# Optimization experiments

Measured on AMD Instinct MI355X. Metric: run time of the kernel, lower is better.

## Reference

```python
import jax, jax.numpy as jnp
import numpy as np

EPS = 1e-12
BIG_NEG = 1e10
SPARSE_RATIO = 0.5
ATTN_W = 0.8
KEEPED = 39          # int(196 * 0.4 * 0.5)
HIDDEN = 102         # int(512 * 0.2)
DIM = 512


def l2norm(x, axis=-1):
    n = jnp.sqrt(jnp.sum(x * x, axis=axis, keepdims=True))
    return x / jnp.maximum(n, EPS)


def layernorm(x, g, b):
    mu = jnp.mean(x, axis=-1, keepdims=True)
    var = jnp.mean(jnp.square(x - mu), axis=-1, keepdims=True)
    return (x - mu) / jnp.sqrt(var + 1e-5) * g + b


def token_aggregation(x, ln_g, ln_b, W1, b1, W2, b2, scale):
    # x: [B, L, C] -> [B, K, C]
    h = layernorm(x, ln_g, ln_b)
    h = jax.nn.gelu(h @ W1 + b1, approximate=False)
    w = h @ W2 + b2                       # [B, L, K]
    w = jnp.swapaxes(w, 1, 2) * scale     # [B, K, L]
    w = jax.nn.softmax(w, axis=2)
    return jnp.einsum('bkl,blc->bkc', w, x)


def setup_inputs() -> dict:
    key = jax.random.key(0)
    ks = jax.random.split(key, 8)
    B_v, L_v, B_t, L_t = 256, 197, 256, 64
    inp = {
        'img_embs': jax.random.normal(ks[0], (B_v, L_v, DIM), jnp.float32),
        'cap_embs': jax.random.normal(ks[1], (B_t, L_t, DIM), jnp.float32),
        'cap_lens': jax.random.randint(ks[2], (B_t,), 8, L_t + 1),
        'ln_g': jnp.ones((DIM,), jnp.float32),
        'ln_b': jnp.zeros((DIM,), jnp.float32),
        'W1': jax.random.normal(ks[3], (DIM, HIDDEN), jnp.float32) * 0.02,
        'b1': jnp.zeros((HIDDEN,), jnp.float32),
        'W2': jax.random.normal(ks[4], (HIDDEN, KEEPED), jnp.float32) * 0.02,
        'b2': jnp.zeros((KEEPED,), jnp.float32),
        'scale': jnp.ones((1, 1, 1), jnp.float32),
    }
    return inp


def reference(img_embs, cap_embs, cap_lens, ln_g, ln_b, W1, b1, W2, b2, scale):
    B_v = img_embs.shape[0]
    L_t = cap_embs.shape[1]
    num_keep = int(KEEPED * SPARSE_RATIO)  # 19

    # CLS split (197 is not a perfect square -> has_cls_token)
    img_cls = img_embs[:, 0:1, :]
    spatial = img_embs[:, 1:, :]

    aggr = token_aggregation(spatial, ln_g, ln_b, W1, b1, W2, b2, scale)  # [B_v, 39, C]
    aggr_norm = l2norm(aggr)
    cap_norm = l2norm(cap_embs)

    glo = jax.lax.stop_gradient(l2norm(jnp.mean(aggr, axis=1, keepdims=True)))
    att_self = jax.lax.stop_gradient(jnp.sum(glo * aggr_norm, axis=-1))  # [B_v, 39]

    word_mask = (jnp.arange(L_t)[None, :] < cap_lens[:, None]).astype(img_embs.dtype)

    def one_caption(cap_i, cap_i_norm, m):
        nw = jnp.sum(m)
        cap_glo = jax.lax.stop_gradient(
            l2norm(jnp.sum(cap_i * m[:, None], axis=0) / nw))        # [C]
        att_y = jax.lax.stop_gradient(
            jnp.sum(cap_glo * aggr_norm, axis=-1))                    # [B_v, 39]
        score = ATTN_W * att_y + (1.0 - ATTN_W) * att_self
        _, idx = jax.lax.top_k(score, num_keep)                       # [B_v, 19]
        select = jnp.take_along_axis(aggr, idx[:, :, None], axis=1)   # [B_v, 19, C]
        score_mask = jnp.zeros_like(score).at[
            jnp.arange(B_v)[:, None], idx].set(1.0)                   # [B_v, 39]
        w_drop = jax.nn.softmax(score - score_mask * BIG_NEG, axis=-1)
        extra = jnp.einsum('bl,blc->bc', w_drop, aggr)[:, None, :]    # [B_v, 1, C]
        sel = l2norm(jnp.concatenate([img_cls, select, extra], axis=1))  # [B_v, 21, C]
        sim = jnp.einsum('wc,bkc->bwk', cap_i_norm, sel)              # [B_v, L_t, 21]
        sim_max = jnp.max(sim, axis=-1)                               # [B_v, L_t]
        sim_text = jnp.sum(sim_max * m, axis=-1) / nw                 # [B_v]
        return sim_text, score_mask

    sims, score_mask_all = jax.vmap(one_caption)(cap_embs, cap_norm, word_mask)
    return sims.T  # [B_v, B_t]
```

## Files before the change

### kernel.cpp

```cpp
#include <hip/hip_runtime.h>
#include <hip/hip_bf16.h>
#include <cfloat>
#include <cmath>

typedef float f32x4 __attribute__((ext_vector_type(4)));
typedef float f32x2 __attribute__((ext_vector_type(2)));
typedef short bf16x8 __attribute__((ext_vector_type(8)));

#define HID 102
#define KEEPN 39
#define DIMD 512

static __device__ __forceinline__ unsigned int f2bf(float v) {
  unsigned int b = __float_as_uint(v);
  return (b + 0x7FFFu + ((b >> 16) & 1u)) >> 16;
}
static __device__ __forceinline__ float wsum(float v) {
#pragma unroll
  for (int m = 1; m < 64; m <<= 1) v += __shfl_xor(v, m, 64);
  return v;
}
static __device__ __forceinline__ float wmaxr(float v) {
#pragma unroll
  for (int m = 1; m < 64; m <<= 1) v = fmaxf(v, __shfl_xor(v, m, 64));
  return v;
}
static __device__ __forceinline__ float bsum(float v, float* red4, int lane, int wid) {
  v = wsum(v);
  if (lane == 0) red4[wid] = v;
  __syncthreads();
  float r = red4[0] + red4[1] + red4[2] + red4[3];
  __syncthreads();
  return r;
}

__global__ __launch_bounds__(256) void k0_prep(
    const float* __restrict__ W1, const float* __restrict__ b1,
    const float* __restrict__ W2, const float* __restrict__ lng,
    const float* __restrict__ lnb,
    float* __restrict__ w1gT, float* __restrict__ b1eff, float* __restrict__ w2T) {
  int tid = blockIdx.x * 256 + threadIdx.x;
  for (int idx = tid; idx < HID * DIMD; idx += (int)gridDim.x * 256) {
    int c = idx >> 9, k = idx & 511;
    w1gT[idx] = lng[k] * W1[k * HID + c];
  }
  for (int idx = tid; idx < KEEPN * 104; idx += (int)gridDim.x * 256) {
    int l = idx / 104, k = idx - l * 104;
    w2T[idx] = (k < HID) ? W2[k * KEEPN + l] : 0.0f;
  }
  if (blockIdx.x == 0 && threadIdx.x < 104) {
    int c = threadIdx.x;
    float s = 0.f;
    if (c < HID) {
      s = b1[c];
      for (int k = 0; k < DIMD; ++k) s += lnb[k] * W1[k * HID + c];
    }
    b1eff[c] = s;
  }
}

__global__ __launch_bounds__(256, 2) void k1a(
    const float* __restrict__ img, const float* __restrict__ w1gT,
    const float* __restrict__ b1eff, const float* __restrict__ w2T,
    const float* __restrict__ b2, const float* __restrict__ scale,
    float* __restrict__ wmat) {
  int b = blockIdx.x;
  int tid = threadIdx.x;
  int lane = tid & 63, wid = tid >> 6;
  __shared__ float mu_s[196], rs_s[196];
  __shared__ __attribute__((aligned(16))) float w2t_s[KEEPN * 104];
  __shared__ float b1e_s[104];
  __shared__ __attribute__((aligned(16))) float uni[6864];
  float* x_s = uni;
  float* w1g_s = uni + 2176;
  float* h1_s = uni;
  const float* xb = img + (size_t)b * 197 * DIMD + DIMD;
  float scv = scale[0];
  for (int u = tid; u < KEEPN * 104 / 4; u += 256)
    ((f32x4*)w2t_s)[u] = ((const f32x4*)w2T)[u];
  if (tid < 104) b1e_s[tid] = b1eff[tid];
#pragma unroll 1
  for (int it = 0; it < 49; ++it) {
    int t = it * 4 + wid;
    const float* xr = xb + (size_t)t * DIMD + lane * 8;
    f32x4 v0 = *(const f32x4*)xr;
    f32x4 v1 = *(const f32x4*)(xr + 4);
    float s = v0[0]+v0[1]+v0[2]+v0[3]+v1[0]+v1[1]+v1[2]+v1[3];
    float q = v0[0]*v0[0]+v0[1]*v0[1]+v0[2]*v0[2]+v0[3]*v0[3]
            + v1[0]*v1[0]+v1[1]*v1[1]+v1[2]*v1[2]+v1[3]*v1[3];
    s = wsum(s); q = wsum(q);
    if (lane == 0) {
      float mu = s * (1.f/512.f);
      float var = q * (1.f/512.f) - mu*mu;
      mu_s[t] = mu;
      rs_s[t] = 1.f / sqrtf(var + 1e-5f);
    }
  }
  __syncthreads();
  int kh = tid >> 7, r = tid & 127, tg = r & 15, cg = r >> 4;
#pragma unroll 1
  for (int t0 = 0; t0 < 196; t0 += 64) {
    float acc[4][13] = {};
#pragma unroll 1
    for (int kc = 0; kc < DIMD; kc += 32) {
      __syncthreads();
#pragma unroll
      for (int j = 0; j < 2; ++j) {
        int u = tid + 256 * j;
        int tt = u >> 3, f = u & 7;
        int t = t0 + tt;
        if (t < 196) {
          f32x4 v = *(const f32x4*)(xb + (size_t)t * DIMD + kc + 4*f);
          float mu = mu_s[t], rs = rs_s[t];
          x_s[(4*f+0)*68 + tt] = (v[0]-mu)*rs;
          x_s[(4*f+1)*68 + tt] = (v[1]-mu)*rs;
          x_s[(4*f+2)*68 + tt] = (v[2]-mu)*rs;
          x_s[(4*f+3)*68 + tt] = (v[3]-mu)*rs;
        }
      }
#pragma unroll
      for (int j = 0; j < 4; ++j) {
        int u = tid + 256 * j;
        if (u < 816) {
          int c = u >> 3, f = u & 7;
          *(f32x4*)&w1g_s[c*36 + 4*f] = *(const f32x4*)(w1gT + c*DIMD + kc + 4*f);
        }
      }
      __syncthreads();
#pragma unroll
      for (int k4 = 0; k4 < 4; ++k4) {
        int kk = kh*16 + k4*4;
        f32x4 a0 = *(const f32x4*)&x_s[(kk+0)*68 + 4*tg];
        f32x4 a1 = *(const f32x4*)&x_s[(kk+1)*68 + 4*tg];
        f32x4 a2 = *(const f32x4*)&x_s[(kk+2)*68 + 4*tg];
        f32x4 a3 = *(const f32x4*)&x_s[(kk+3)*68 + 4*tg];
#pragma unroll
        for (int ci = 0; ci < 13; ++ci) {
          f32x4 w = *(const f32x4*)&w1g_s[(cg*13+ci)*36 + kk];
#pragma unroll
          for (int t = 0; t < 4; ++t)
            acc[t][ci] += a0[t]*w[0] + a1[t]*w[1] + a2[t]*w[2] + a3[t]*w[3];
        }
      }
    }
    __syncthreads();
    if (kh == 1) {
#pragma unroll
      for (int ci = 0; ci < 13; ++ci) {
        int c = cg*13 + ci;
        if (c < HID)
#pragma unroll
          for (int t = 0; t < 4; ++t) h1_s[c*66 + 4*tg + t] = acc[t][ci];
      }
    }
    __syncthreads();
    if (kh == 0) {
#pragma unroll
      for (int ci = 0; ci < 13; ++ci) {
        int c = cg*13 + ci;
        if (c < HID)
#pragma unroll
          for (int t = 0; t < 4; ++t) {
            float v = h1_s[c*66 + 4*tg + t] + acc[t][ci] + b1e_s[c];
            v = 0.5f * v * (1.f + erff(v * 0.70710678118654752f));
            h1_s[c*66 + 4*tg + t] = v;
          }
      }
    }
    if (tid < 128) h1_s[(HID + (tid >> 6))*66 + (tid & 63)] = 0.f;
    __syncthreads();
    {
      int t4 = tid & 31, lg = tid >> 5;
      int nl = (lg == 7) ? 4 : 5;
      float a2c[2][5] = {};
#pragma unroll 2
      for (int k = 0; k < 104; k += 4) {
        f32x4 wvv[5];
#pragma unroll
        for (int li = 0; li < 5; ++li) {
          if (li < nl) wvv[li] = *(const f32x4*)&w2t_s[(lg*5+li)*104 + k];
          else wvv[li] = (f32x4){0.f,0.f,0.f,0.f};
        }
#pragma unroll
        for (int j = 0; j < 4; ++j) {
          f32x2 h = *(const f32x2*)&h1_s[(k+j)*66 + 2*t4];
#pragma unroll
          for (int li = 0; li < 5; ++li) {
            a2c[0][li] += h[0]*wvv[li][j];
            a2c[1][li] += h[1]*wvv[li][j];
          }
        }
      }
#pragma unroll
      for (int li = 0; li < 5; ++li) {
        if (li < nl) {
          int l = lg*5 + li;
          float bb = b2[l];
#pragma unroll
          for (int tp = 0; tp < 2; ++tp) {
            int t = t0 + 2*t4 + tp;
            if (t < 196) wmat[((size_t)b*KEEPN + l)*196 + t] = (a2c[tp][li] + bb) * scv;
          }
        }
      }
    }
  }
}

__global__ __launch_bounds__(256) void k1agg(
    const float* __restrict__ img, const float* __restrict__ wmat,
    float* __restrict__ agn, unsigned short* __restrict__ bm,
    float* __restrict__ na_g, float* __restrict__ gloraw) {
  int b = blockIdx.x, tid = threadIdx.x;
  int lane = tid & 63, wid = tid >> 6;
  __shared__ __attribute__((aligned(16))) float wm_s[KEEPN * 200];
  __shared__ float red_s[13 * 4];
  __shared__ float na_s[13];
  for (int u = tid; u < KEEPN * 49; u += 256) {
    int l = u / 49, t4 = u - l * 49;
    *(f32x4*)&wm_s[l*200 + 4*t4] = *(const f32x4*)(wmat + ((size_t)b*KEEPN + l)*196 + 4*t4);
  }
  __syncthreads();
  for (int l = wid; l < KEEPN; l += 4) {
    float v0 = wm_s[l*200 + lane];
    float v1 = wm_s[l*200 + 64 + lane];
    float v2 = wm_s[l*200 + 128 + lane];
    float v3 = (lane < 4) ? wm_s[l*200 + 192 + lane] : -FLT_MAX;
    float mx = wmaxr(fmaxf(fmaxf(v0, v1), fmaxf(v2, v3)));
    float e0 = expf(v0 - mx), e1 = expf(v1 - mx), e2 = expf(v2 - mx);
    float e3 = (lane < 4) ? expf(v3 - mx) : 0.f;
    float s = wsum(e0 + e1 + e2 + e3);
    float inv = 1.f / s;
    wm_s[l*200 + lane] = e0 * inv;
    wm_s[l*200 + 64 + lane] = e1 * inv;
    wm_s[l*200 + 128 + lane] = e2 * inv;
    if (lane < 4) wm_s[l*200 + 192 + lane] = e3 * inv;
  }
  __syncthreads();
  const float* xb = img + (size_t)b * 197 * DIMD + DIMD;
  int cc = 2 * tid;
  float ms0 = 0.f, ms1 = 0.f;
#pragma unroll 1
  for (int lp = 0; lp < 3; ++lp) {
    int l0 = lp * 13;
    float a0[13] = {}, a1[13] = {};
#pragma unroll 1
    for (int t4 = 0; t4 < 49; ++t4) {
      f32x2 xx[4];
#pragma unroll
      for (int j = 0; j < 4; ++j) {
        int t = 4*t4 + j;
        xx[j] = *(const f32x2*)(xb + (size_t)t*DIMD + cc);
      }
#pragma unroll
      for (int li = 0; li < 13; ++li) {
        f32x4 w = *(const f32x4*)&wm_s[(l0+li)*200 + 4*t4];
#pragma unroll
        for (int j = 0; j < 4; ++j) {
          a0[li] += w[j]*xx[j][0];
          a1[li] += w[j]*xx[j][1];
        }
      }
    }
#pragma unroll
    for (int li = 0; li < 13; ++li) {
      float p = wsum(a0[li]*a0[li] + a1[li]*a1[li]);
      if (lane == 0) red_s[li*4 + wid] = p;
    }
    __syncthreads();
    if (tid < 13) {
      float s = red_s[tid*4] + red_s[tid*4+1] + red_s[tid*4+2] + red_s[tid*4+3];
      float n = sqrtf(s);
      na_s[tid] = n;
      na_g[b*KEEPN + l0 + tid] = n;
    }
    __syncthreads();
#pragma unroll
    for (int li = 0; li < 13; ++li) {
      int l = l0 + li;
      float inv = 1.f / fmaxf(na_s[li], 1e-12f);
      size_t abase = ((size_t)b*KEEPN + l) * DIMD;
      size_t bbase = ((size_t)b*48 + l) * DIMD;
      float v0 = a0[li]*inv, v1 = a1[li]*inv;
      *(f32x2*)&agn[abase + cc] = (f32x2){v0, v1};
      *(unsigned int*)&bm[bbase + cc] = f2bf(v0) | (f2bf(v1) << 16);
      ms0 += a0[li]; ms1 += a1[li];
    }
    __syncthreads();
  }
  *(f32x2*)&gloraw[(size_t)b*DIMD + cc] = (f32x2){ms0, ms1};
}

__global__ __launch_bounds__(256) void k1b(
    const float* __restrict__ img, const float* __restrict__ gloraw,
    const float* __restrict__ agn, const float* __restrict__ na_g,
    unsigned short* __restrict__ bm, float* __restrict__ attSelf,
    float* __restrict__ G) {
  int b = blockIdx.x, tid = threadIdx.x;
  int lane = tid & 63, wid = tid >> 6;
  __shared__ float glo_s[DIMD];
  __shared__ float red4[4];
  int c0 = tid, c1 = tid + 256;
  float m0 = gloraw[(size_t)b*DIMD + c0] * (1.f/39.f);
  float m1 = gloraw[(size_t)b*DIMD + c1] * (1.f/39.f);
  float nt = bsum(m0*m0 + m1*m1, red4, lane, wid);
  float inv = 1.f / fmaxf(sqrtf(nt), 1e-12f);
  glo_s[c0] = m0*inv; glo_s[c1] = m1*inv;
  const float* cls = img + (size_t)b * 197 * DIMD;
  float x0 = cls[c0], x1 = cls[c1];
  float n2 = bsum(x0*x0 + x1*x1, red4, lane, wid);
  float inv2 = 1.f / fmaxf(sqrtf(n2), 1e-12f);
  bm[((size_t)b*48 + 39)*DIMD + c0] = (unsigned short)f2bf(x0*inv2);
  bm[((size_t)b*48 + 39)*DIMD + c1] = (unsigned short)f2bf(x1*inv2);
  for (int u = tid; u < 8*DIMD; u += 256) {
    int rr = u >> 9, c = u & 511;
    bm[((size_t)b*48 + 40 + rr)*DIMD + c] = 0;
  }
  __syncthreads();
#pragma unroll 1
  for (int l = wid; l < KEEPN; l += 4) {
    const float* ar = agn + ((size_t)b*KEEPN + l)*DIMD + lane*8;
    const float* gp = glo_s + lane*8;
    f32x4 a0 = *(const f32x4*)ar;
    f32x4 a1 = *(const f32x4*)(ar + 4);
    f32x4 g0 = *(const f32x4*)gp;
    f32x4 g1 = *(const f32x4*)(gp + 4);
    float p = a0[0]*g0[0]+a0[1]*g0[1]+a0[2]*g0[2]+a0[3]*g0[3]
            + a1[0]*g1[0]+a1[1]*g1[1]+a1[2]*g1[2]+a1[3]*g1[3];
    p = wsum(p);
    if (lane == 0) attSelf[b*KEEPN + l] = p;
  }
#pragma unroll 1
  for (int p = tid; p < KEEPN*KEEPN; p += 256) {
    int l = p / KEEPN, lq = p - l*KEEPN;
    const float* A = agn + ((size_t)b*KEEPN + l)*DIMD;
    const float* B = agn + ((size_t)b*KEEPN + lq)*DIMD;
    float d = 0.f;
#pragma unroll 4
    for (int c = 0; c < DIMD; c += 4) {
      f32x4 va = *(const f32x4*)(A + c);
      f32x4 vb = *(const f32x4*)(B + c);
      d += va[0]*vb[0] + va[1]*vb[1] + va[2]*vb[2] + va[3]*vb[3];
    }
    G[(size_t)b*(KEEPN*KEEPN) + p] = d * na_g[b*KEEPN + l] * na_g[b*KEEPN + lq];
  }
}

__global__ __launch_bounds__(256) void k2(
    const float* __restrict__ cap, const int* __restrict__ lens,
    unsigned short* __restrict__ capn_bf, float* __restrict__ cglo) {
  int i = blockIdx.x, tid = threadIdx.x;
  int lane = tid & 63, wid = tid >> 6;
  __shared__ float red4[4];
  int len = lens[i];
  float nwf = (float)len;
  const float* cb = cap + (size_t)i * 64 * DIMD;
  for (int w = wid; w < 64; w += 4) {
    const float* xr = cb + (size_t)w*DIMD + lane*8;
    f32x4 v0 = *(const f32x4*)xr;
    f32x4 v1 = *(const f32x4*)(xr + 4);
    float q = v0[0]*v0[0]+v0[1]*v0[1]+v0[2]*v0[2]+v0[3]*v0[3]
            + v1[0]*v1[0]+v1[1]*v1[1]+v1[2]*v1[2]+v1[3]*v1[3];
    q = wsum(q);
    float inv = 1.f / fmaxf(sqrtf(q), 1e-12f);
    uint4 o;
    o.x = f2bf(v0[0]*inv) | (f2bf(v0[1]*inv) << 16);
    o.y = f2bf(v0[2]*inv) | (f2bf(v0[3]*inv) << 16);
    o.z = f2bf(v1[0]*inv) | (f2bf(v1[1]*inv) << 16);
    o.w = f2bf(v1[2]*inv) | (f2bf(v1[3]*inv) << 16);
    *(uint4*)(capn_bf + ((size_t)i*64 + w)*DIMD + lane*8) = o;
  }
  int c0 = tid, c1 = tid + 256;
  float s0 = 0.f, s1 = 0.f;
#pragma unroll 1
  for (int w = 0; w < len; ++w) {
    s0 += cb[(size_t)w*DIMD + c0];
    s1 += cb[(size_t)w*DIMD + c1];
  }
  s0 /= nwf; s1 /= nwf;
  float nt = bsum(s0*s0 + s1*s1, red4, lane, wid);
  float inv = 1.f / fmaxf(sqrtf(nt), 1e-12f);
  cglo[(size_t)i*DIMD + c0] = s0*inv;
  cglo[(size_t)i*DIMD + c1] = s1*inv;
}

__global__ __launch_bounds__(256) void k3p(
    const float* __restrict__ agn, const float* __restrict__ cglo,
    const float* __restrict__ attSelf, const float* __restrict__ na_g,
    const float* __restrict__ G,
    float* __restrict__ wdna_g, unsigned long long* __restrict__ selmask_g,
    float* __restrict__ nexinv_g) {
  int b = blockIdx.x, igrp = blockIdx.y;
  int tid = threadIdx.x, lane = tid & 63, wv = tid >> 6;
  __shared__ __attribute__((aligned(16))) float cg_s[64*36];
  __shared__ __attribute__((aligned(16))) float ag_s[40*36];
  __shared__ float sc_s[64*40];
  __shared__ float G_s[39*33];
  __shared__ float as_s[40];
  __shared__ float na_s[40];
  int ic0 = igrp * 64;
  for (int u = tid; u < KEEPN*KEEPN; u += 256) {
    int l = u / 39, q = u - l*39;
    G_s[l*33 + q] = G[(size_t)b*(KEEPN*KEEPN) + u];
  }
  if (tid < 39) { as_s[tid] = attSelf[b*KEEPN + tid]; na_s[tid] = na_g[b*KEEPN + tid]; }
  int i2 = tid & 31, l5 = tid >> 5;
  float acc0[5] = {}, acc1[5] = {};
#pragma unroll 1
  for (int kc = 0; kc < DIMD; kc += 32) {
    __syncthreads();
#pragma unroll
    for (int j = 0; j < 2; ++j) {
      int idx = tid + 256*j;
      int r = idx >> 3, cq = idx & 7;
      *(f32x4*)&cg_s[r*36 + 4*cq] = *(const f32x4*)&cglo[(size_t)(ic0 + r)*DIMD + kc + 4*cq];
    }
    if (tid < 320) {
      int r = tid >> 3, cq = tid & 7;
      f32x4 v = {0.f,0.f,0.f,0.f};
      if (r < 39) v = *(const f32x4*)&agn[((size_t)b*KEEPN + r)*DIMD + kc + 4*cq];
      *(f32x4*)&ag_s[r*36 + 4*cq] = v;
    }
    __syncthreads();
#pragma unroll
    for (int c4 = 0; c4 < 8; ++c4) {
      f32x4 a0 = *(const f32x4*)&cg_s[i2*36 + 4*c4];
      f32x4 a1 = *(const f32x4*)&cg_s[(i2+32)*36 + 4*c4];
#pragma unroll
      for (int li = 0; li < 5; ++li) {
        f32x4 bv = *(const f32x4*)&ag_s[(l5*5+li)*36 + 4*c4];
        acc0[li] += a0[0]*bv[0]+a0[1]*bv[1]+a0[2]*bv[2]+a0[3]*bv[3];
        acc1[li] += a1[0]*bv[0]+a1[1]*bv[1]+a1[2]*bv[2]+a1[3]*bv[3];
      }
    }
  }
  __syncthreads();
#pragma unroll
  for (int li = 0; li < 5; ++li) {
    int l = l5*5 + li;
    if (l < KEEPN) {
      sc_s[i2*40 + l]      = 0.8f*acc0[li] + 0.2f*as_s[l];
      sc_s[(i2+32)*40 + l] = 0.8f*acc1[li] + 0.2f*as_s[l];
    }
  }
  __syncthreads();
#pragma unroll 1
  for (int it = 0; it < 16; ++it) {
    int ic = it*4 + wv;
    size_t pair = (size_t)b*256 + ic0 + ic;
    float sc = (lane < KEEPN) ? sc_s[ic*40 + lane] : -FLT_MAX;
    int rank = 0;
    for (int lp = 0; lp < KEEPN; ++lp) {
      float ov = __shfl(sc, lp, 64);
      if (ov > sc || (ov == sc && lp < lane)) rank++;
    }
    bool selected = (lane < KEEPN && rank < 19);
    float uv = (lane < KEEPN && !selected) ? sc : -FLT_MAX;
    float m2 = wmaxr(uv);
    float pp = (lane < KEEPN && !selected) ? expf(sc - m2) : 0.f;
    float S = wsum(pp);
    float wd = pp / S;
    float rowdot = 0.f;
    for (int lp = 0; lp < KEEPN; ++lp) {
      float wdlp = __shfl(wd, lp, 64);
      if (lane < KEEPN) rowdot += wdlp * G_s[lane*33 + lp];
    }
    float nex2 = wsum((lane < KEEPN) ? wd*rowdot : 0.f);
    unsigned long long msk = __ballot(selected) | (1ull << 39);
    if (lane < 40) wdna_g[pair*40 + lane] = (lane < KEEPN) ? wd * na_s[lane] : 0.f;
    if (lane == 0) {
      selmask_g[pair] = msk;
      nexinv_g[pair] = 1.f / fmaxf(sqrtf(fmaxf(nex2, 0.f)), 1e-12f);
    }
  }
}

__global__ __launch_bounds__(256, 2) void k3g(
    const unsigned short* __restrict__ capn_bf, const unsigned short* __restrict__ bm,
    const float* __restrict__ wdna_g, const unsigned long long* __restrict__ selmask_g,
    const float* __restrict__ nexinv_g, const int* __restrict__ lens,
    float* __restrict__ out) {
  int bid = blockIdx.x;
  int btile = bid >> 8;
  int i = bid & 255;
  int tid = threadIdx.x, lane = tid & 63, wv = tid >> 6;
  __shared__ __attribute__((aligned(16))) unsigned short A_s[2][64*64];
  __shared__ float wd_s[8*48];
  __shared__ float sf_s[8*48];
  __shared__ float nx_s[8];
  int len = lens[i];
  const unsigned short* cb = capn_bf + (size_t)i * 64 * DIMD;
  const unsigned short* bb = bm + (size_t)btile * 384 * DIMD;
  for (int u = tid; u < 384; u += 256) {
    int g = u / 48, l = u - g*48;
    size_t pair = (size_t)(btile*8 + g)*256 + i;
    float wdv = 0.f, sfv = 0.f;
    if (l < 40) {
      wdv = wdna_g[pair*40 + l];
      sfv = ((selmask_g[pair] >> l) & 1ull) ? 1.f : 0.f;
    }
    wd_s[u] = wdv; sf_s[u] = sfv;
    if (l == 0) nx_s[g] = nexinv_g[pair];
  }
  int srow = tid >> 3, sk8 = tid & 7;
  int sdst0 = srow*64 + (sk8 ^ (srow & 7))*8;
  int sdst1 = (srow+32)*64 + (sk8 ^ (srow & 7))*8;
  {
    uint4 v0 = *(const uint4*)(cb + (size_t)srow*DIMD + sk8*8);
    uint4 v1 = *(const uint4*)(cb + (size_t)(srow+32)*DIMD + sk8*8);
    *(uint4*)&A_s[0][sdst0] = v0;
    *(uint4*)&A_s[0][sdst1] = v1;
  }
  f32x4 acc[4][6];
#pragma unroll
  for (int m = 0; m < 4; ++m)
#pragma unroll
    for (int n = 0; n < 6; ++n) acc[m][n] = (f32x4){0.f,0.f,0.f,0.f};
  __syncthreads();
  int cur = 0;
#pragma unroll 1
  for (int kc = 0; kc < 8; ++kc) {
    uint4 sv0, sv1;
    if (kc < 7) {
      sv0 = *(const uint4*)(cb + (size_t)srow*DIMD + (kc+1)*64 + sk8*8);
      sv1 = *(const uint4*)(cb + (size_t)(srow+32)*DIMD + (kc+1)*64 + sk8*8);
    }
#pragma unroll
    for (int ks = 0; ks < 2; ++ks) {
      int kh = 4*ks + (lane >> 4);
      bf16x8 af[4], bfr[6];
#pragma unroll
      for (int n = 0; n < 6; ++n) {
        int row = 16*(6*wv + n) + (lane & 15);
        bfr[n] = *(const bf16x8*)(bb + (size_t)row*DIMD + kc*64 + kh*8);
      }
#pragma unroll
      for (int m = 0; m < 4; ++m) {
        int row = 16*m + (lane & 15);
        af[m] = *(const bf16x8*)&A_s[cur][row*64 + (kh ^ (row & 7))*8];
      }
#pragma unroll
      for (int m = 0; m < 4; ++m)
#pragma unroll
        for (int n = 0; n < 6; ++n)
          acc[m][n] = __builtin_amdgcn_mfma_f32_16x16x32_bf16(af[m], bfr[n], acc[m][n], 0, 0, 0);
    }
    if (kc < 7) {
      *(uint4*)&A_s[cur ^ 1][sdst0] = sv0;
      *(uint4*)&A_s[cur ^ 1][sdst1] = sv1;
    }
    __syncthreads();
    cur ^= 1;
  }
  float pv[2] = {0.f, 0.f};
#pragma unroll
  for (int jj = 0; jj < 2; ++jj) {
    int g = 2*wv + jj;
    float nxi = nx_s[g];
#pragma unroll
    for (int m = 0; m < 4; ++m) {
      f32x4 ed = {0.f,0.f,0.f,0.f};
      f32x4 ms = {-FLT_MAX,-FLT_MAX,-FLT_MAX,-FLT_MAX};
#pragma unroll
      for (int j = 0; j < 3; ++j) {
        int l = 16*j + (lane & 15);
        float wdv = wd_s[g*48 + l];
        float sfv = sf_s[g*48 + l];
        f32x4 v = acc[m][3*jj + j];
#pragma unroll
        for (int q = 0; q < 4; ++q) {
          ed[q] += wdv * v[q];
          ms[q] = fmaxf(ms[q], (sfv > 0.5f) ? v[q] : -FLT_MAX);
        }
      }
#pragma unroll
      for (int sh = 1; sh < 16; sh <<= 1) {
#pragma unroll
        for (int q = 0; q < 4; ++q) {
          ed[q] += __shfl_xor(ed[q], sh, 64);
          ms[q] = fmaxf(ms[q], __shfl_xor(ms[q], sh, 64));
        }
      }
      if ((lane & 15) == 0) {
#pragma unroll
        for (int q = 0; q < 4; ++q) {
          int r2 = 16*m + (lane >> 4)*4 + q;
          float smax = fmaxf(ms[q], ed[q]*nxi);
          pv[jj] += (r2 < len) ? smax : 0.f;
        }
      }
    }
    pv[jj] += __shfl_xor(pv[jj], 16, 64);
    pv[jj] += __shfl_xor(pv[jj], 32, 64);
  }
  if (lane == 0) {
#pragma unroll
    for (int jj = 0; jj < 2; ++jj) {
      int g = 2*wv + jj;
      out[(size_t)(btile*8 + g)*256 + i] = pv[jj] / (float)len;
    }
  }
}

extern "C" void kernel_launch(void* const* d_in, const int* in_sizes, int n_in,
                              void* d_out, int out_size, void* d_ws, size_t ws_size,
                              hipStream_t stream) {
  const float* img = (const float*)d_in[0];
  const float* cap = (const float*)d_in[1];
  const int* lens = (const int*)d_in[2];
  const float* lng = (const float*)d_in[3];
  const float* lnb = (const float*)d_in[4];
  const float* W1 = (const float*)d_in[5];
  const float* b1 = (const float*)d_in[6];
  const float* W2 = (const float*)d_in[7];
  const float* b2 = (const float*)d_in[8];
  const float* scale = (const float*)d_in[9];
  float* out = (float*)d_out;
  char* ws = (char*)d_ws;
  size_t off = 0;
  auto alloc = [&](size_t bytes) -> void* {
    void* p = ws + off;
    off += (bytes + 255) & ~(size_t)255;
    return p;
  };
  float* agn             = (float*)alloc((size_t)256*39*512*4);
  unsigned short* bm     = (unsigned short*)alloc((size_t)256*48*512*2);
  unsigned short* capn_bf = (unsigned short*)alloc((size_t)256*64*512*2);
  float* cglo    = (float*)alloc((size_t)256*512*4);
  float* gloraw  = (float*)alloc((size_t)256*512*4);
  float* na_g    = (float*)alloc((size_t)256*39*4);
  float* attSelf = (float*)alloc((size_t)256*39*4);
  float* G       = (float*)alloc((size_t)256*39*39*4);
  float* w1gT    = (float*)alloc((size_t)102*512*4);
  float* b1eff   = (float*)alloc((size_t)104*4);
  float* w2T     = (float*)alloc((size_t)39*104*4);
  float* wmat    = (float*)alloc((size_t)256*39*196*4);
  float* wdna_g  = (float*)alloc((size_t)65536*40*4);
  unsigned long long* selmask_g = (unsigned long long*)alloc((size_t)65536*8);
  float* nexinv_g = (float*)alloc((size_t)65536*4);
  (void)in_sizes; (void)n_in; (void)out_size; (void)ws_size;

  hipLaunchKernelGGL(k0_prep, dim3(64), dim3(256), 0, stream,
                     W1, b1, W2, lng, lnb, w1gT, b1eff, w2T);
  hipLaunchKernelGGL(k1a, dim3(256), dim3(256), 0, stream,
                     img, w1gT, b1eff, w2T, b2, scale, wmat);
  hipLaunchKernelGGL(k1agg, dim3(256), dim3(256), 0, stream,
                     img, wmat, agn, bm, na_g, gloraw);
  hipLaunchKernelGGL(k1b, dim3(256), dim3(256), 0, stream,
                     img, gloraw, agn, na_g, bm, attSelf, G);
  hipLaunchKernelGGL(k2, dim3(256), dim3(256), 0, stream,
                     cap, lens, capn_bf, cglo);
  hipLaunchKernelGGL(k3p, dim3(256, 4), dim3(256), 0, stream,
                     agn, cglo, attSelf, na_g, G, wdna_g, selmask_g, nexinv_g);
  hipLaunchKernelGGL(k3g, dim3(8192), dim3(256), 0, stream,
                     capn_bf, bm, wdna_g, selmask_g, nexinv_g, lens, out);
}
```

Measured before the change: 1.321 ms.

## Stage B tile in LDS, process two captions per block, single-pass aggregation

k3g now runs 512-thread blocks that each handle two captions and stage both the caption tile and the shared 384-row image tile in LDS, instead of each wave reading B fragments straight from global memory. This lets the image tile be reused across two captions, at the cost of dropping the register double-buffering and adding two barriers per k-chunk. k1agg also accumulates all 39 aggregated tokens in one pass over the image rows instead of three passes of 13, so each image is read once. The price is about 78 accumulator registers per thread, which may lower occupancy.

```diff
diff --git a/kernel.cpp b/kernel.cpp
--- a/kernel.cpp
+++ b/kernel.cpp
@@ -214,8 +214,8 @@
   int b = blockIdx.x, tid = threadIdx.x;
   int lane = tid & 63, wid = tid >> 6;
   __shared__ __attribute__((aligned(16))) float wm_s[KEEPN * 200];
-  __shared__ float red_s[13 * 4];
-  __shared__ float na_s[13];
+  __shared__ float red_s[KEEPN * 4];
+  __shared__ float na_s[KEEPN];
   for (int u = tid; u < KEEPN * 49; u += 256) {
     int l = u / 49, t4 = u - l * 49;
     *(f32x4*)&wm_s[l*200 + 4*t4] = *(const f32x4*)(wmat + ((size_t)b*KEEPN + l)*196 + 4*t4);
@@ -239,54 +239,45 @@
   __syncthreads();
   const float* xb = img + (size_t)b * 197 * DIMD + DIMD;
   int cc = 2 * tid;
+  float a0[KEEPN], a1[KEEPN];
+#pragma unroll
+  for (int li = 0; li < KEEPN; ++li) { a0[li] = 0.f; a1[li] = 0.f; }
+#pragma unroll 1
+  for (int t4 = 0; t4 < 49; ++t4) {
+    f32x2 x0 = *(const f32x2*)(xb + (size_t)(4*t4+0)*DIMD + cc);
+    f32x2 x1 = *(const f32x2*)(xb + (size_t)(4*t4+1)*DIMD + cc);
+    f32x2 x2 = *(const f32x2*)(xb + (size_t)(4*t4+2)*DIMD + cc);
+    f32x2 x3 = *(const f32x2*)(xb + (size_t)(4*t4+3)*DIMD + cc);
+#pragma unroll
+    for (int li = 0; li < KEEPN; ++li) {
+      f32x4 w = *(const f32x4*)&wm_s[li*200 + 4*t4];
+      a0[li] += w[0]*x0[0] + w[1]*x1[0] + w[2]*x2[0] + w[3]*x3[0];
+      a1[li] += w[0]*x0[1] + w[1]*x1[1] + w[2]*x2[1] + w[3]*x3[1];
+    }
+  }
+#pragma unroll
+  for (int li = 0; li < KEEPN; ++li) {
+    float p = wsum(a0[li]*a0[li] + a1[li]*a1[li]);
+    if (lane == 0) red_s[li*4 + wid] = p;
+  }
+  __syncthreads();
+  if (tid < KEEPN) {
+    float s = red_s[tid*4] + red_s[tid*4+1] + red_s[tid*4+2] + red_s[tid*4+3];
+    float n = sqrtf(s);
+    na_s[tid] = n;
+    na_g[b*KEEPN + tid] = n;
+  }
+  __syncthreads();
   float ms0 = 0.f, ms1 = 0.f;
-#pragma unroll 1
-  for (int lp = 0; lp < 3; ++lp) {
-    int l0 = lp * 13;
-    float a0[13] = {}, a1[13] = {};
-#pragma unroll 1
-    for (int t4 = 0; t4 < 49; ++t4) {
-      f32x2 xx[4];
-#pragma unroll
-      for (int j = 0; j < 4; ++j) {
-        int t = 4*t4 + j;
-        xx[j] = *(const f32x2*)(xb + (size_t)t*DIMD + cc);
-      }
-#pragma unroll
-      for (int li = 0; li < 13; ++li) {
-        f32x4 w = *(const f32x4*)&wm_s[(l0+li)*200 + 4*t4];
-#pragma unroll
-        for (int j = 0; j < 4; ++j) {
-          a0[li] += w[j]*xx[j][0];
-          a1[li] += w[j]*xx[j][1];
-        }
-      }
-    }
-#pragma unroll
-    for (int li = 0; li < 13; ++li) {
-      float p = wsum(a0[li]*a0[li] + a1[li]*a1[li]);
-      if (lane == 0) red_s[li*4 + wid] = p;
-    }
-    __syncthreads();
-    if (tid < 13) {
-      float s = red_s[tid*4] + red_s[tid*4+1] + red_s[tid*4+2] + red_s[tid*4+3];
-      float n = sqrtf(s);
-      na_s[tid] = n;
-      na_g[b*KEEPN + l0 + tid] = n;
-    }
-    __syncthreads();
-#pragma unroll
-    for (int li = 0; li < 13; ++li) {
-      int l = l0 + li;
-      float inv = 1.f / fmaxf(na_s[li], 1e-12f);
-      size_t abase = ((size_t)b*KEEPN + l) * DIMD;
-      size_t bbase = ((size_t)b*48 + l) * DIMD;
-      float v0 = a0[li]*inv, v1 = a1[li]*inv;
-      *(f32x2*)&agn[abase + cc] = (f32x2){v0, v1};
-      *(unsigned int*)&bm[bbase + cc] = f2bf(v0) | (f2bf(v1) << 16);
-      ms0 += a0[li]; ms1 += a1[li];
-    }
-    __syncthreads();
+#pragma unroll
+  for (int li = 0; li < KEEPN; ++li) {
+    float inv = 1.f / fmaxf(na_s[li], 1e-12f);
+    size_t abase = ((size_t)b*KEEPN + li) * DIMD;
+    size_t bbase = ((size_t)b*48 + li) * DIMD;
+    float v0 = a0[li]*inv, v1 = a1[li]*inv;
+    *(f32x2*)&agn[abase + cc] = (f32x2){v0, v1};
+    *(unsigned int*)&bm[bbase + cc] = f2bf(v0) | (f2bf(v1) << 16);
+    ms0 += a0[li]; ms1 += a1[li];
   }
   *(f32x2*)&gloraw[(size_t)b*DIMD + cc] = (f32x2){ms0, ms1};
 }
@@ -475,69 +466,76 @@
   }
 }
 
-__global__ __launch_bounds__(256, 2) void k3g(
+__global__ __launch_bounds__(512) void k3g(
     const unsigned short* __restrict__ capn_bf, const unsigned short* __restrict__ bm,
     const float* __restrict__ wdna_g, const unsigned long long* __restrict__ selmask_g,
     const float* __restrict__ nexinv_g, const int* __restrict__ lens,
     float* __restrict__ out) {
   int bid = blockIdx.x;
-  int btile = bid >> 8;
-  int i = bid & 255;
+  int btile = bid >> 7;
+  int i0 = (bid & 127) * 2;
   int tid = threadIdx.x, lane = tid & 63, wv = tid >> 6;
-  __shared__ __attribute__((aligned(16))) unsigned short A_s[2][64*64];
-  __shared__ float wd_s[8*48];
-  __shared__ float sf_s[8*48];
-  __shared__ float nx_s[8];
-  int len = lens[i];
-  const unsigned short* cb = capn_bf + (size_t)i * 64 * DIMD;
-  const unsigned short* bb = bm + (size_t)btile * 384 * DIMD;
-  for (int u = tid; u < 384; u += 256) {
-    int g = u / 48, l = u - g*48;
-    size_t pair = (size_t)(btile*8 + g)*256 + i;
+  __shared__ __attribute__((aligned(16))) unsigned short A_s[128*64];
+  __shared__ __attribute__((aligned(16))) unsigned short B_s[384*64];
+  __shared__ float wd_s[16*48];
+  __shared__ float sf_s[16*48];
+  __shared__ float nx_s[16];
+  const unsigned short* cb0 = capn_bf + (size_t)i0 * 64 * DIMD;
+  const unsigned short* bb  = bm + (size_t)btile * 384 * DIMD;
+  for (int u = tid; u < 768; u += 512) {
+    int pc = u / 48, l = u - pc*48;
+    int g = pc >> 1, ci = pc & 1;
+    size_t pair = (size_t)(btile*8 + g)*256 + (i0 + ci);
     float wdv = 0.f, sfv = 0.f;
     if (l < 40) {
       wdv = wdna_g[pair*40 + l];
       sfv = ((selmask_g[pair] >> l) & 1ull) ? 1.f : 0.f;
     }
     wd_s[u] = wdv; sf_s[u] = sfv;
-    if (l == 0) nx_s[g] = nexinv_g[pair];
-  }
-  int srow = tid >> 3, sk8 = tid & 7;
-  int sdst0 = srow*64 + (sk8 ^ (srow & 7))*8;
-  int sdst1 = (srow+32)*64 + (sk8 ^ (srow & 7))*8;
-  {
-    uint4 v0 = *(const uint4*)(cb + (size_t)srow*DIMD + sk8*8);
-    uint4 v1 = *(const uint4*)(cb + (size_t)(srow+32)*DIMD + sk8*8);
-    *(uint4*)&A_s[0][sdst0] = v0;
-    *(uint4*)&A_s[0][sdst1] = v1;
-  }
+    if (l == 0) nx_s[pc] = nexinv_g[pair];
+  }
+  int cw = wv & 1, gg = wv >> 1;
+  int lenc = lens[i0 + cw];
   f32x4 acc[4][6];
 #pragma unroll
   for (int m = 0; m < 4; ++m)
 #pragma unroll
     for (int n = 0; n < 6; ++n) acc[m][n] = (f32x4){0.f,0.f,0.f,0.f};
-  __syncthreads();
-  int cur = 0;
 #pragma unroll 1
   for (int kc = 0; kc < 8; ++kc) {
-    uint4 sv0, sv1;
-    if (kc < 7) {
-      sv0 = *(const uint4*)(cb + (size_t)srow*DIMD + (kc+1)*64 + sk8*8);
-      sv1 = *(const uint4*)(cb + (size_t)(srow+32)*DIMD + (kc+1)*64 + sk8*8);
-    }
+    __syncthreads();
+#pragma unroll
+    for (int half = 0; half < 2; ++half) {
+      uint4 v4[4];
+#pragma unroll
+      for (int j = 0; j < 4; ++j) {
+        int u = (half*4 + j)*512 + tid;
+        const unsigned short* src;
+        if (u < 1024) { int row = u >> 3, k8 = u & 7; src = cb0 + (size_t)row*DIMD + kc*64 + k8*8; }
+        else { int ub = u - 1024; int row = ub >> 3, k8 = ub & 7; src = bb + (size_t)row*DIMD + kc*64 + k8*8; }
+        v4[j] = *(const uint4*)src;
+      }
+#pragma unroll
+      for (int j = 0; j < 4; ++j) {
+        int u = (half*4 + j)*512 + tid;
+        if (u < 1024) { int row = u >> 3, k8 = u & 7; *(uint4*)&A_s[row*64 + (k8 ^ (row&7))*8] = v4[j]; }
+        else { int ub = u - 1024; int row = ub >> 3, k8 = ub & 7; *(uint4*)&B_s[row*64 + (k8 ^ (row&7))*8] = v4[j]; }
+      }
+    }
+    __syncthreads();
 #pragma unroll
     for (int ks = 0; ks < 2; ++ks) {
       int kh = 4*ks + (lane >> 4);
       bf16x8 af[4], bfr[6];
 #pragma unroll
+      for (int m = 0; m < 4; ++m) {
+        int row = 64*cw + 16*m + (lane & 15);
+        af[m] = *(const bf16x8*)&A_s[row*64 + (kh ^ (row & 7))*8];
+      }
+#pragma unroll
       for (int n = 0; n < 6; ++n) {
-        int row = 16*(6*wv + n) + (lane & 15);
-        bfr[n] = *(const bf16x8*)(bb + (size_t)row*DIMD + kc*64 + kh*8);
-      }
-#pragma unroll
-      for (int m = 0; m < 4; ++m) {
-        int row = 16*m + (lane & 15);
-        af[m] = *(const bf16x8*)&A_s[cur][row*64 + (kh ^ (row & 7))*8];
+        int row = 16*(6*gg + n) + (lane & 15);
+        bfr[n] = *(const bf16x8*)&B_s[row*64 + (kh ^ (row & 7))*8];
       }
 #pragma unroll
       for (int m = 0; m < 4; ++m)
@@ -545,18 +543,13 @@
         for (int n = 0; n < 6; ++n)
           acc[m][n] = __builtin_amdgcn_mfma_f32_16x16x32_bf16(af[m], bfr[n], acc[m][n], 0, 0, 0);
     }
-    if (kc < 7) {
-      *(uint4*)&A_s[cur ^ 1][sdst0] = sv0;
-      *(uint4*)&A_s[cur ^ 1][sdst1] = sv1;
-    }
-    __syncthreads();
-    cur ^= 1;
   }
   float pv[2] = {0.f, 0.f};
 #pragma unroll
   for (int jj = 0; jj < 2; ++jj) {
-    int g = 2*wv + jj;
-    float nxi = nx_s[g];
+    int g = 2*gg + jj;
+    int pc = g*2 + cw;
+    float nxi = nx_s[pc];
 #pragma unroll
     for (int m = 0; m < 4; ++m) {
       f32x4 ed = {0.f,0.f,0.f,0.f};
@@ -564,8 +557,8 @@
 #pragma unroll
       for (int j = 0; j < 3; ++j) {
         int l = 16*j + (lane & 15);
-        float wdv = wd_s[g*48 + l];
-        float sfv = sf_s[g*48 + l];
+        float wdv = wd_s[pc*48 + l];
+        float sfv = sf_s[pc*48 + l];
         f32x4 v = acc[m][3*jj + j];
 #pragma unroll
         for (int q = 0; q < 4; ++q) {
@@ -586,7 +579,7 @@
         for (int q = 0; q < 4; ++q) {
           int r2 = 16*m + (lane >> 4)*4 + q;
           float smax = fmaxf(ms[q], ed[q]*nxi);
-          pv[jj] += (r2 < len) ? smax : 0.f;
+          pv[jj] += (r2 < lenc) ? smax : 0.f;
         }
       }
     }
@@ -596,8 +589,8 @@
   if (lane == 0) {
 #pragma unroll
     for (int jj = 0; jj < 2; ++jj) {
-      int g = 2*wv + jj;
-      out[(size_t)(btile*8 + g)*256 + i] = pv[jj] / (float)len;
+      int g = 2*gg + jj;
+      out[(size_t)(btile*8 + g)*256 + (i0 + cw)] = pv[jj] / (float)lenc;
     }
   }
 }
@@ -652,6 +645,6 @@
                      cap, lens, capn_bf, cglo);
   hipLaunchKernelGGL(k3p, dim3(256, 4), dim3(256), 0, stream,
                      agn, cglo, attSelf, na_g, G, wdna_g, selmask_g, nexinv_g);
-  hipLaunchKernelGGL(k3g, dim3(8192), dim3(256), 0, stream,
+  hipLaunchKernelGGL(k3g, dim3(4096), dim3(512), 0, stream,
                      capn_bf, bm, wdna_g, selmask_g, nexinv_g, lens, out);
 }
```

Measured after the change: 1.302 ms. No clear change (-1.4%).
